# Kernel tuning notes

Hardware: AMD Instinct MI355X
Metric: run time of the kernel (lower is better)

Reference implementation:

```python
import jax, jax.numpy as jnp
import numpy as np

B, S0 = 16, 511
D = 512    # encoder_output_dim
HG = 256   # graph_rnn_hidden_graph
HE = 256   # graph_rnn_hidden_edge (must equal HG: h_prev[0] = graph_state)
T = 128    # tag_representation_dim
M = 32     # graph_rnn_m
S = S0 + 1 # after head-sentinel prepend


def setup_inputs() -> dict:
    ks = iter(jax.random.split(jax.random.key(0), 40))
    def U(shape, fan):
        # torch RNN/Linear default init: U(-1/sqrt(fan), 1/sqrt(fan))
        return jax.random.uniform(next(ks), shape, jnp.float32, -1.0, 1.0) / np.sqrt(fan)
    return {
        'input': jax.random.normal(next(ks), (B, S0, D), jnp.float32),
        'sentinel': jax.random.normal(next(ks), (D,), jnp.float32),
        'g_Wih0': U((HG, D), HG), 'g_Whh0': U((HG, HG), HG), 'g_bih0': U((HG,), HG), 'g_bhh0': U((HG,), HG),
        'g_Wih1': U((HG, HG), HG), 'g_Whh1': U((HG, HG), HG), 'g_bih1': U((HG,), HG), 'g_bhh1': U((HG,), HG),
        'e_Wih0': U((HE, 1), HE), 'e_Whh0': U((HE, HE), HE), 'e_bih0': U((HE,), HE), 'e_bhh0': U((HE,), HE),
        'e_Wih1': U((HE, HE), HE), 'e_Whh1': U((HE, HE), HE), 'e_bih1': U((HE,), HE), 'e_bhh1': U((HE,), HE),
        'cls_W': U((1, HE), HE), 'cls_b': U((1,), HE),
        'head_W': U((T, HG), HG), 'head_b': U((T,), HG),
        'dep_W': U((T, HG), HG), 'dep_b': U((T,), HG),
        'mask': jnp.ones((B, S0), jnp.int32),
        'head_indices': jax.random.randint(next(ks), (B, S0), 0, S0, jnp.int32),
    }


def _rnn_layer(x, W_ih, W_hh, b_ih, b_hh):
    # Elman RNN layer (tanh), batch_first, h0 = 0. x: [B, S, Din] -> [B, S, H]
    xw = jnp.einsum('bsd,hd->bsh', x, W_ih) + b_ih + b_hh  # hoist input GEMM out of scan
    h0 = jnp.zeros((x.shape[0], W_hh.shape[0]), x.dtype)
    def step(h, xw_t):
        h = jnp.tanh(xw_t + h @ W_hh.T)
        return h, h
    _, ys = jax.lax.scan(step, h0, jnp.swapaxes(xw, 0, 1))
    return jnp.swapaxes(ys, 0, 1)


def _forward(input, sentinel, g_Wih0, g_Whh0, g_bih0, g_bhh0, g_Wih1, g_Whh1, g_bih1, g_bhh1,
             e_Wih0, e_Whh0, e_bih0, e_bhh0, e_Wih1, e_Whh1, e_bih1, e_bhh1,
             cls_W, cls_b, head_W, head_b, dep_W, dep_b, mask, head_indices):
    Bv = input.shape[0]
    # prepend head sentinel / prepend_ones
    x = jnp.concatenate([jnp.broadcast_to(sentinel, (Bv, 1, D)), input], axis=1)   # [B,S,D]
    mask_f = jnp.concatenate([jnp.ones((Bv, 1), mask.dtype), mask], axis=1)        # [B,S]
    # graph_pass: 2-layer tanh RNN; pad_packed_sequence zeroes padded timesteps
    h = _rnn_layer(x, g_Wih0, g_Whh0, g_bih0, g_bhh0)
    gs = _rnn_layer(h, g_Wih1, g_Whh1, g_bih1, g_bhh1)                             # [B,S,HG]
    gs = gs * mask_f[..., None].astype(gs.dtype)
    N = Bv * S
    gt = gs.reshape(N, HG)
    def estep(carry, _):
        xe, h0, h1 = carry
        h0 = jnp.tanh(xe @ e_Wih0.T + e_bih0 + e_bhh0 + h0 @ e_Whh0.T)
        h1 = jnp.tanh(h0 @ e_Wih1.T + e_bih1 + e_bhh1 + h1 @ e_Whh1.T)
        p = jax.nn.sigmoid(h1 @ cls_W.T + cls_b)   # [N,1]
        return (p, h0, h1), p[:, 0]
    init = (jnp.ones((N, 1), gs.dtype), gt, jnp.zeros((N, HE), gs.dtype))
    _, probs = jax.lax.scan(estep, init, None, length=M)                           # [M,N]
    A = jnp.concatenate([jnp.ones((1, N), gs.dtype), probs], axis=0).T.reshape(Bv, S, M + 1)
    # reshape_adj: scatter the M-band back into a [B,S,S] matrix, then transpose
    Ab = A[:, :, 1:]                                                               # [B,S,M]
    i = jnp.arange(S)[:, None]
    j = jnp.arange(S)[None, :]
    start = jnp.maximum(0, i - M)
    valid = (j >= start) & (j < i)
    midx = jnp.clip(j - start, 0, M - 1)                                           # [S,S]
    gathered = Ab[:, jnp.arange(S)[:, None], midx]                                 # [B,S,S]
    arc_logits = jnp.swapaxes(jnp.where(valid[None], gathered, jnp.zeros((), gs.dtype)), 1, 2)
    # tag heads (dropout = identity at inference)
    head_tag = jax.nn.elu(jnp.einsum('bsh,th->bst', gs, head_W) + head_b)
    dep_tag = jax.nn.elu(jnp.einsum('bsh,th->bst', gs, dep_W) + dep_b)
    return head_tag, dep_tag, arc_logits


def reference(input, sentinel, g_Wih0, g_Whh0, g_bih0, g_bhh0, g_Wih1, g_Whh1, g_bih1, g_bhh1,
              e_Wih0, e_Whh0, e_bih0, e_bhh0, e_Wih1, e_Whh1, e_bih1, e_bhh1,
              cls_W, cls_b, head_W, head_b, dep_W, dep_b, mask, head_indices):
    return _forward(input, sentinel, g_Wih0, g_Whh0, g_bih0, g_bhh0, g_Wih1, g_Whh1, g_bih1, g_bhh1,
                    e_Wih0, e_Whh0, e_bih0, e_bhh0, e_Wih1, e_Whh1, e_bih1, e_bhh1,
                    cls_W, cls_b, head_W, head_b, dep_W, dep_b, mask, head_indices)
```

## Files before the change

kernel.cpp:

```cpp
#include <hip/hip_runtime.h>

typedef unsigned short u16;
typedef short s8v __attribute__((ext_vector_type(8)));
typedef float f4v __attribute__((ext_vector_type(4)));

__device__ __forceinline__ float bf2f(u16 s) {
  unsigned u = ((unsigned)s) << 16;
  return __builtin_bit_cast(float, u);
}
__device__ __forceinline__ u16 f2bf(float f) {
  unsigned u = __builtin_bit_cast(unsigned, f);
  unsigned r = u + 0x7fffu + ((u >> 16) & 1u);
  return (u16)(r >> 16);
}
__device__ __forceinline__ s8v load8bf(const u16* p) {
  return __builtin_bit_cast(s8v, *(const uint4*)p);
}
__device__ __forceinline__ f4v mfma16(s8v a, s8v b, f4v c) {
  return __builtin_amdgcn_mfma_f32_16x16x32_bf16(a, b, c, 0, 0, 0);
}
__device__ __forceinline__ s8v pin8(s8v x) {
  union { s8v v; unsigned u[4]; } t;
  t.v = x;
  asm volatile("" : "+v"(t.u[0]), "+v"(t.u[1]), "+v"(t.u[2]), "+v"(t.u[3]));
  return t.v;
}
__device__ __forceinline__ void barrier_lds() {
  asm volatile("s_waitcnt lgkmcnt(0)\n\ts_barrier" ::: "memory");
}
__device__ __forceinline__ void cvt8(const float* p, s8v& hi, s8v& lo) {
  float4 x0 = ((const float4*)p)[0];
  float4 x1 = ((const float4*)p)[1];
  float v[8] = {x0.x, x0.y, x0.z, x0.w, x1.x, x1.y, x1.z, x1.w};
  union { s8v v; u16 a[8]; } H, L;
#pragma unroll
  for (int i = 0; i < 8; ++i) {
    u16 h = f2bf(v[i]);
    H.a[i] = h;
    L.a[i] = f2bf(v[i] - bf2f(h));
  }
  hi = H.v;
  lo = L.v;
}
__device__ __forceinline__ float fast_tanh(float x) {
  float t = __builtin_amdgcn_exp2f(x * 2.885390081777927f);
  return 1.f - 2.f * __builtin_amdgcn_rcpf(t + 1.f);
}
__device__ __forceinline__ float fast_sigmoid(float x) {
  float t = __builtin_amdgcn_exp2f(x * -1.4426950408889634f);
  return __builtin_amdgcn_rcpf(1.f + t);
}

__global__ void k_prep(const float* __restrict__ W0, const float* __restrict__ W1,
                       u16* __restrict__ whh0b, u16* __restrict__ whh1b,
                       const float* __restrict__ E0, const float* __restrict__ E1,
                       const float* __restrict__ E2, u16* __restrict__ B0,
                       u16* __restrict__ B1, u16* __restrict__ B2,
                       const float* __restrict__ gW0, u16* __restrict__ gw0hi,
                       u16* __restrict__ gw0lo, const float* __restrict__ gW1,
                       u16* __restrict__ gw1hi, u16* __restrict__ gw1lo,
                       const float* __restrict__ hW, u16* __restrict__ hWhi,
                       u16* __restrict__ hWlo, const float* __restrict__ dW,
                       u16* __restrict__ dWhi, u16* __restrict__ dWlo,
                       const int* __restrict__ mask, float* __restrict__ maskfb) {
  int t = blockIdx.x * 256 + threadIdx.x;
  if (t < 131072) {
    int layer = t >> 16;
    int idx = t & 65535;
    const float* W = layer ? W1 : W0;
    u16* dst = layer ? whh1b : whh0b;
    dst[idx] = f2bf(W[idx]);
  } else if (t < 327680) {
    int c = t - 131072;
    int which = c >> 16;
    int idx = c & 65535;
    const float* src = which == 0 ? E0 : (which == 1 ? E1 : E2);
    u16* dst = which == 0 ? B0 : (which == 1 ? B1 : B2);
    dst[idx] = f2bf(src[idx]);
  } else if (t < 589824) {
    const float* src;
    u16 *dhi, *dlo;
    int idx;
    if (t < 458752) { idx = t - 327680; src = gW0; dhi = gw0hi; dlo = gw0lo; }
    else if (t < 524288) { idx = t - 458752; src = gW1; dhi = gw1hi; dlo = gw1lo; }
    else if (t < 557056) { idx = t - 524288; src = hW; dhi = hWhi; dlo = hWlo; }
    else { idx = t - 557056; src = dW; dhi = dWhi; dlo = dWlo; }
    float v = src[idx];
    u16 h = f2bf(v);
    dhi[idx] = h;
    dlo[idx] = f2bf(v - bf2f(h));
  } else if (t < 598016) {
    int c = t - 589824;
    int s = c >> 4, b = c & 15;
    maskfb[c] = (s == 0) ? 1.f : (float)mask[b * 511 + s - 1];
  }
}

__launch_bounds__(256)
__global__ void k_xw0(const float* __restrict__ input, const float* __restrict__ sentinel,
                      const u16* __restrict__ Whi, const u16* __restrict__ Wlo,
                      const float* __restrict__ b1, const float* __restrict__ b2,
                      float* __restrict__ outxw) {
  const int l = threadIdx.x & 63;
  const int wv = threadIdx.x >> 6;
  const int l15 = l & 15, q = l >> 4;
  const int row0 = blockIdx.x * 64 + wv * 16;
  const int col0 = blockIdx.y * 64;
  int row = row0 + l15;
  int s = row & 511, b = row >> 9;
  const float* aptr = (s == 0) ? sentinel : input + (((size_t)(b * 511 + s - 1)) << 9);
  f4v acc[4];
#pragma unroll
  for (int i = 0; i < 4; ++i) acc[i] = (f4v){0.f, 0.f, 0.f, 0.f};
#pragma unroll
  for (int kt = 0; kt < 16; ++kt) {
    int k0 = kt * 32 + q * 8;
    s8v ah, al;
    cvt8(aptr + k0, ah, al);
#pragma unroll
    for (int nt = 0; nt < 4; ++nt) {
      int j = col0 + nt * 16 + l15;
      s8v wh = load8bf(Whi + ((size_t)j << 9) + k0);
      s8v wl = load8bf(Wlo + ((size_t)j << 9) + k0);
      acc[nt] = mfma16(ah, wh, acc[nt]);
      acc[nt] = mfma16(al, wh, acc[nt]);
      acc[nt] = mfma16(ah, wl, acc[nt]);
    }
  }
#pragma unroll
  for (int nt = 0; nt < 4; ++nt) {
    int col = col0 + nt * 16 + l15;
    float bias = b1[col] + b2[col];
#pragma unroll
    for (int r = 0; r < 4; ++r) {
      int rr = row0 + q * 4 + r;
      outxw[((size_t)rr << 8) + col] = acc[nt][r] + bias;
    }
  }
}

__launch_bounds__(256)
__global__ void k_gemm2(const float* __restrict__ A,
                        const u16* __restrict__ WhiA, const u16* __restrict__ WloA,
                        const float* __restrict__ bA, float* __restrict__ outA,
                        const u16* __restrict__ WhiB, const u16* __restrict__ WloB,
                        const float* __restrict__ bB, float* __restrict__ outB,
                        int K, int J) {
  const u16* Whi = blockIdx.z ? WhiB : WhiA;
  const u16* Wlo = blockIdx.z ? WloB : WloA;
  const float* b1 = blockIdx.z ? bB : bA;
  float* outf = blockIdx.z ? outB : outA;
  const int l = threadIdx.x & 63;
  const int wv = threadIdx.x >> 6;
  const int l15 = l & 15, q = l >> 4;
  const int row0 = blockIdx.x * 64 + wv * 16;
  const int col0 = blockIdx.y * 64;
  const float* aptr = A + (size_t)(row0 + l15) * K;
  f4v acc[4];
#pragma unroll
  for (int i = 0; i < 4; ++i) acc[i] = (f4v){0.f, 0.f, 0.f, 0.f};
  const int nkt = K >> 5;
  for (int kt = 0; kt < nkt; ++kt) {
    int k0 = kt * 32 + q * 8;
    s8v ah, al;
    cvt8(aptr + k0, ah, al);
#pragma unroll
    for (int nt = 0; nt < 4; ++nt) {
      int j = col0 + nt * 16 + l15;
      s8v wh = load8bf(Whi + (size_t)j * K + k0);
      s8v wl = load8bf(Wlo + (size_t)j * K + k0);
      acc[nt] = mfma16(ah, wh, acc[nt]);
      acc[nt] = mfma16(al, wh, acc[nt]);
      acc[nt] = mfma16(ah, wl, acc[nt]);
    }
  }
#pragma unroll
  for (int nt = 0; nt < 4; ++nt) {
    int col = col0 + nt * 16 + l15;
    float bias = b1[col];
#pragma unroll
    for (int r = 0; r < 4; ++r) {
      int rr = row0 + q * 4 + r;
      float v = acc[nt][r] + bias;
      v = v > 0.f ? v : (__builtin_amdgcn_exp2f(v * 1.4426950408889634f) - 1.f);
      outf[(size_t)rr * J + col] = v;
    }
  }
}

__launch_bounds__(512, 2)
__global__ void k_scan_f(const float* __restrict__ xw, const u16* __restrict__ W0b,
                         const u16* __restrict__ Wxb, const u16* __restrict__ W1b,
                         const float* __restrict__ bih1, const float* __restrict__ bhh1,
                         float* __restrict__ outf, const float* __restrict__ maskf) {
  __shared__ u16 H1[2][272];
  __shared__ u16 H2[2][272];
  __shared__ float XW2[2][272];
  __shared__ float mtab[512];
  const int tid = threadIdx.x;
  const int l = tid & 63, wv = tid >> 6;
  const int l15 = l & 15, q = l >> 4;
  const int b = blockIdx.x;

  s8v w0[2][8], wx[2][8], w1[2][8];
#pragma unroll
  for (int nt = 0; nt < 2; ++nt) {
    int j = wv * 32 + nt * 16 + l15;
#pragma unroll
    for (int kt = 0; kt < 8; ++kt) {
      int off = (j << 8) + kt * 32 + q * 8;
      w0[nt][kt] = pin8(load8bf(W0b + off));
      wx[nt][kt] = pin8(load8bf(Wxb + off));
      w1[nt][kt] = pin8(load8bf(W1b + off));
    }
  }
  if (tid < 256) {
    H1[0][tid] = 0; H1[1][tid] = 0;
    H2[0][tid] = 0; H2[1][tid] = 0;
    XW2[0][tid] = 0.f; XW2[1][tid] = 0.f;
  }
  if (tid < 512) mtab[tid] = maskf[tid * 16 + b];

  const int j0 = wv * 32 + l15;
  float b2v[2];
#pragma unroll
  for (int nt = 0; nt < 2; ++nt) b2v[nt] = bih1[j0 + nt * 16] + bhh1[j0 + nt * 16];
  __syncthreads();

  const size_t nbase = (size_t)b << 9;
  const float* xrow = xw + (nbase << 8);
  const int q0 = (q == 0);

  float xA[2], xB[2];
#pragma unroll
  for (int nt = 0; nt < 2; ++nt) {
    xA[nt] = xrow[j0 + nt * 16];
    xB[nt] = xrow[256 + j0 + nt * 16];
  }

  auto STEP = [&](int g, int par, float* xc) {
    const u16* H1r = &H1[par][0];
    const u16* H2r = &H2[par][0];
    f4v a1[2], ax[2], a2[2], a2b[2];
#pragma unroll
    for (int nt = 0; nt < 2; ++nt) {
      a1[nt] = (f4v){xc[nt], 0.f, 0.f, 0.f};
      ax[nt] = (f4v){b2v[nt], 0.f, 0.f, 0.f};
      a2[nt] = (f4v){XW2[par][j0 + nt * 16], 0.f, 0.f, 0.f};
      a2b[nt] = (f4v){0.f, 0.f, 0.f, 0.f};
    }
#pragma unroll
    for (int kt = 0; kt < 8; ++kt) {
      s8v h1b = load8bf(H1r + kt * 32 + q * 8);
#pragma unroll
      for (int nt = 0; nt < 2; ++nt) {
        a1[nt] = mfma16(h1b, w0[nt][kt], a1[nt]);
        ax[nt] = mfma16(h1b, wx[nt][kt], ax[nt]);
      }
    }
    if (g < 512) {
      u16* Hw = &H1[1 - par][0];
#pragma unroll
      for (int nt = 0; nt < 2; ++nt) {
        float h = fast_tanh(a1[nt][0]);
        if (q0) Hw[j0 + nt * 16] = f2bf(h);
      }
    }
    if (g >= 1 && g < 513) {
      float* Xw = &XW2[1 - par][0];
#pragma unroll
      for (int nt = 0; nt < 2; ++nt)
        if (q0) Xw[j0 + nt * 16] = ax[nt][0];
    }
#pragma unroll
    for (int kt = 0; kt < 8; ++kt) {
      s8v h2b = load8bf(H2r + kt * 32 + q * 8);
#pragma unroll
      for (int nt = 0; nt < 2; ++nt) {
        if (kt & 1) a2b[nt] = mfma16(h2b, w1[nt][kt], a2b[nt]);
        else        a2[nt]  = mfma16(h2b, w1[nt][kt], a2[nt]);
      }
    }
    if (g >= 2) {
      int t = g - 2;
      float mf = mtab[t];
      u16* Hw = &H2[1 - par][0];
      float* orow = outf + ((nbase + t) << 8);
#pragma unroll
      for (int nt = 0; nt < 2; ++nt) {
        float h = fast_tanh(a2[nt][0] + a2b[nt][0]);
        if (q0) {
          Hw[j0 + nt * 16] = f2bf(h);
          orow[j0 + nt * 16] = h * mf;
        }
      }
    }
  };

  for (int g = 0; g < 514; g += 2) {
    STEP(g, 0, xA);
    int sp = g + 2; if (sp > 511) sp = 511;
#pragma unroll
    for (int nt = 0; nt < 2; ++nt) xA[nt] = xrow[(sp << 8) + j0 + nt * 16];
    barrier_lds();
    STEP(g + 1, 1, xB);
    int sq = g + 3; if (sq > 511) sq = 511;
#pragma unroll
    for (int nt = 0; nt < 2; ++nt) xB[nt] = xrow[(sq << 8) + j0 + nt * 16];
    barrier_lds();
  }
}

__launch_bounds__(512, 2)
__global__ void k_enc(const float* __restrict__ gs,
                      const u16* __restrict__ W0b, const u16* __restrict__ W1b,
                      const u16* __restrict__ W2b, const float* __restrict__ wih0,
                      const float* __restrict__ bih0, const float* __restrict__ bhh0,
                      const float* __restrict__ bih1, const float* __restrict__ bhh1,
                      const float* __restrict__ clsW, const float* __restrict__ clsb,
                      float* __restrict__ Ab) {
  __shared__ __align__(16) u16 hA0[32 * 264];
  __shared__ __align__(16) u16 hA1[32 * 264];
  __shared__ float xe[32];
  __shared__ float b0v[256], w0v[256], b1v[256], clsv[256];
  __shared__ float clsbs;
  const int tid = threadIdx.x;
  const int n0 = blockIdx.x * 32;

  for (int c = tid; c < 8192; c += 512) {
    int row = c >> 8, col = c & 255;
    hA0[row * 264 + col] = f2bf(gs[(((size_t)(n0 + row)) << 8) + col]);
    hA1[row * 264 + col] = 0;
  }
  if (tid < 256) {
    b0v[tid] = bih0[tid] + bhh0[tid];
    w0v[tid] = wih0[tid];
    b1v[tid] = bih1[tid] + bhh1[tid];
    clsv[tid] = clsW[tid];
  }
  if (tid < 32) xe[tid] = 1.0f;
  if (tid == 0) clsbs = clsb[0];

  const int l = tid & 63, wv = tid >> 6;
  const int l15 = l & 15, q = l >> 4;
  const int colbase = wv * 32;

  s8v w0[2][8], w1[2][8], w2[2][8];
#pragma unroll
  for (int nt = 0; nt < 2; ++nt) {
    int jj = colbase + nt * 16 + l15;
#pragma unroll
    for (int kt = 0; kt < 8; ++kt) {
      int off = (jj << 8) + kt * 32 + q * 8;
      w0[nt][kt] = load8bf(W0b + off);
      w1[nt][kt] = load8bf(W1b + off);
      w2[nt][kt] = load8bf(W2b + off);
    }
  }
  __syncthreads();

  for (int m = 0; m < 32; ++m) {
    f4v acc[2][2];
#pragma unroll
    for (int mt = 0; mt < 2; ++mt)
#pragma unroll
      for (int nt = 0; nt < 2; ++nt) acc[mt][nt] = (f4v){0.f, 0.f, 0.f, 0.f};
#pragma unroll
    for (int kt = 0; kt < 8; ++kt) {
#pragma unroll
      for (int mt = 0; mt < 2; ++mt) {
        s8v a = __builtin_bit_cast(s8v, *(const uint4*)&hA0[(mt * 16 + l15) * 264 + kt * 32 + q * 8]);
        acc[mt][0] = mfma16(a, w0[0][kt], acc[mt][0]);
        acc[mt][1] = mfma16(a, w0[1][kt], acc[mt][1]);
      }
    }
    __syncthreads();
#pragma unroll
    for (int nt = 0; nt < 2; ++nt) {
      int col = colbase + nt * 16 + l15;
      float wc = w0v[col], bc = b0v[col];
#pragma unroll
      for (int mt = 0; mt < 2; ++mt)
#pragma unroll
        for (int r = 0; r < 4; ++r) {
          int row = mt * 16 + q * 4 + r;
          float v = acc[mt][nt][r] + xe[row] * wc + bc;
          hA0[row * 264 + col] = f2bf(fast_tanh(v));
        }
    }
    __syncthreads();
#pragma unroll
    for (int mt = 0; mt < 2; ++mt)
#pragma unroll
      for (int nt = 0; nt < 2; ++nt) acc[mt][nt] = (f4v){0.f, 0.f, 0.f, 0.f};
#pragma unroll
    for (int kt = 0; kt < 8; ++kt) {
#pragma unroll
      for (int mt = 0; mt < 2; ++mt) {
        s8v a0 = __builtin_bit_cast(s8v, *(const uint4*)&hA0[(mt * 16 + l15) * 264 + kt * 32 + q * 8]);
        s8v a1 = __builtin_bit_cast(s8v, *(const uint4*)&hA1[(mt * 16 + l15) * 264 + kt * 32 + q * 8]);
        acc[mt][0] = mfma16(a0, w1[0][kt], acc[mt][0]);
        acc[mt][1] = mfma16(a0, w1[1][kt], acc[mt][1]);
        acc[mt][0] = mfma16(a1, w2[0][kt], acc[mt][0]);
        acc[mt][1] = mfma16(a1, w2[1][kt], acc[mt][1]);
      }
    }
    __syncthreads();
#pragma unroll
    for (int nt = 0; nt < 2; ++nt) {
      int col = colbase + nt * 16 + l15;
      float bc = b1v[col];
#pragma unroll
      for (int mt = 0; mt < 2; ++mt)
#pragma unroll
        for (int r = 0; r < 4; ++r) {
          int row = mt * 16 + q * 4 + r;
          float v = acc[mt][nt][r] + bc;
          hA1[row * 264 + col] = f2bf(fast_tanh(v));
        }
    }
    __syncthreads();
    if (tid < 256) {
      int row = tid >> 3, seg = tid & 7;
      float sum = 0.f;
#pragma unroll
      for (int u = 0; u < 4; ++u) {
        int col = seg * 32 + u * 8;
#pragma unroll
        for (int e = 0; e < 8; ++e) sum += bf2f(hA1[row * 264 + col + e]) * clsv[col + e];
      }
      sum += __shfl_down(sum, 4, 8);
      sum += __shfl_down(sum, 2, 8);
      sum += __shfl_down(sum, 1, 8);
      if (seg == 0) {
        float pp = fast_sigmoid(sum + clsbs);
        xe[row] = pp;
        Ab[(((size_t)(n0 + row)) << 5) + m] = pp;
      }
    }
    __syncthreads();
  }
}

__global__ void k_arc(const float* __restrict__ Ab, float* __restrict__ out2) {
  int t = blockIdx.x * 256 + threadIdx.x;
  int b = t >> 18;
  int rem = t & 262143;
  int j = rem >> 9, i = rem & 511;
  int start = i - 32;
  if (start < 0) start = 0;
  float v = 0.f;
  if (j >= start && j < i) v = Ab[((((size_t)b << 9) + i) << 5) + (j - start)];
  out2[t] = v;
}

extern "C" void kernel_launch(void* const* d_in, const int* in_sizes, int n_in,
                              void* d_out, int out_size, void* d_ws, size_t ws_size,
                              hipStream_t stream) {
  const float* input    = (const float*)d_in[0];
  const float* sentinel = (const float*)d_in[1];
  const float* g_Wih0   = (const float*)d_in[2];
  const float* g_Whh0   = (const float*)d_in[3];
  const float* g_bih0   = (const float*)d_in[4];
  const float* g_bhh0   = (const float*)d_in[5];
  const float* g_Wih1   = (const float*)d_in[6];
  const float* g_Whh1   = (const float*)d_in[7];
  const float* g_bih1   = (const float*)d_in[8];
  const float* g_bhh1   = (const float*)d_in[9];
  const float* e_Wih0   = (const float*)d_in[10];
  const float* e_Whh0   = (const float*)d_in[11];
  const float* e_bih0   = (const float*)d_in[12];
  const float* e_bhh0   = (const float*)d_in[13];
  const float* e_Wih1   = (const float*)d_in[14];
  const float* e_Whh1   = (const float*)d_in[15];
  const float* e_bih1   = (const float*)d_in[16];
  const float* e_bhh1   = (const float*)d_in[17];
  const float* cls_W    = (const float*)d_in[18];
  const float* cls_b    = (const float*)d_in[19];
  const float* head_W   = (const float*)d_in[20];
  const float* head_b   = (const float*)d_in[21];
  const float* dep_W    = (const float*)d_in[22];
  const float* dep_b    = (const float*)d_in[23];
  const int* mask       = (const int*)d_in[24];

  float* out = (float*)d_out;
  char* ws = (char*)d_ws;
  float* xw_buf = (float*)ws;
  float* gsb    = (float*)(ws + (16u << 20));
  float* Ab     = (float*)(ws + (24u << 20));
  size_t o = (25u << 20);
  u16* whh0b   = (u16*)(ws + o); o += 128u << 10;
  u16* whh1b   = (u16*)(ws + o); o += 128u << 10;
  float* maskfb= (float*)(ws + o); o += 32u << 10;
  u16* eb0     = (u16*)(ws + o); o += 128u << 10;
  u16* eb1     = (u16*)(ws + o); o += 128u << 10;
  u16* eb2     = (u16*)(ws + o); o += 128u << 10;
  u16* gw0hi   = (u16*)(ws + o); o += 256u << 10;
  u16* gw0lo   = (u16*)(ws + o); o += 256u << 10;
  u16* gw1hi   = (u16*)(ws + o); o += 128u << 10;
  u16* gw1lo   = (u16*)(ws + o); o += 128u << 10;
  u16* hWhi    = (u16*)(ws + o); o += 64u << 10;
  u16* hWlo    = (u16*)(ws + o); o += 64u << 10;
  u16* dWhi    = (u16*)(ws + o); o += 64u << 10;
  u16* dWlo    = (u16*)(ws + o); o += 64u << 10;

  k_prep<<<2336, 256, 0, stream>>>(g_Whh0, g_Whh1, whh0b, whh1b, e_Whh0, e_Wih1, e_Whh1,
                                   eb0, eb1, eb2, g_Wih0, gw0hi, gw0lo, g_Wih1, gw1hi,
                                   gw1lo, head_W, hWhi, hWlo, dep_W, dWhi, dWlo,
                                   mask, maskfb);
  k_xw0<<<dim3(128, 4), 256, 0, stream>>>(input, sentinel, gw0hi, gw0lo, g_bih0, g_bhh0,
                                          xw_buf);
  k_scan_f<<<16, 512, 0, stream>>>(xw_buf, whh0b, gw1hi, whh1b, g_bih1, g_bhh1,
                                   gsb, maskfb);
  k_gemm2<<<dim3(128, 2, 2), 256, 0, stream>>>(gsb, hWhi, hWlo, head_b, out,
                                               dWhi, dWlo, dep_b, out + 1048576,
                                               256, 128);
  k_enc<<<256, 512, 0, stream>>>(gsb, eb0, eb1, eb2, e_Wih0, e_bih0, e_bhh0,
                                 e_bih1, e_bhh1, cls_W, cls_b, Ab);
  k_arc<<<16384, 256, 0, stream>>>(Ab, out + 2097152);
}
```

Before: 867.7 us.

## Replace MFMA matvec in graph RNN scan with fp16 dot2 lane-pair reductions

```diff
diff --git a/kernel.cpp b/kernel.cpp
--- a/kernel.cpp
+++ b/kernel.cpp
@@ -3,6 +3,9 @@
 typedef unsigned short u16;
 typedef short s8v __attribute__((ext_vector_type(8)));
 typedef float f4v __attribute__((ext_vector_type(4)));
+typedef _Float16 f16;
+typedef _Float16 h2v __attribute__((ext_vector_type(2)));
+typedef _Float16 h8v __attribute__((ext_vector_type(8)));
 
 __device__ __forceinline__ float bf2f(u16 s) {
   unsigned u = ((unsigned)s) << 16;
@@ -19,14 +22,27 @@
 __device__ __forceinline__ f4v mfma16(s8v a, s8v b, f4v c) {
   return __builtin_amdgcn_mfma_f32_16x16x32_bf16(a, b, c, 0, 0, 0);
 }
-__device__ __forceinline__ s8v pin8(s8v x) {
-  union { s8v v; unsigned u[4]; } t;
+__device__ __forceinline__ h8v pinh(h8v x) {
+  union { h8v v; unsigned u[4]; } t;
   t.v = x;
   asm volatile("" : "+v"(t.u[0]), "+v"(t.u[1]), "+v"(t.u[2]), "+v"(t.u[3]));
   return t.v;
 }
 __device__ __forceinline__ void barrier_lds() {
   asm volatile("s_waitcnt lgkmcnt(0)\n\ts_barrier" ::: "memory");
+}
+__device__ __forceinline__ float swz_xor1(float x) {
+  int i = __builtin_bit_cast(int, x);
+  i = __builtin_amdgcn_ds_swizzle(i, 0x041F);
+  return __builtin_bit_cast(float, i);
+}
+__device__ __forceinline__ h2v pr(h8v v, int e) {
+  union { h8v v; h2v p[4]; } t;
+  t.v = v;
+  return t.p[e];
+}
+__device__ __forceinline__ float fdot2(h2v a, h2v b, float c) {
+  return __builtin_amdgcn_fdot2(a, b, c, false);
 }
 __device__ __forceinline__ void cvt8(const float* p, s8v& hi, s8v& lo) {
   float4 x0 = ((const float4*)p)[0];
@@ -51,27 +67,27 @@
   return __builtin_amdgcn_rcpf(1.f + t);
 }
 
-__global__ void k_prep(const float* __restrict__ W0, const float* __restrict__ W1,
-                       u16* __restrict__ whh0b, u16* __restrict__ whh1b,
+__global__ void k_prep(const float* __restrict__ W0, const float* __restrict__ Wx,
+                       const float* __restrict__ W1, f16* __restrict__ w0h,
+                       f16* __restrict__ wxh, f16* __restrict__ w1h,
                        const float* __restrict__ E0, const float* __restrict__ E1,
                        const float* __restrict__ E2, u16* __restrict__ B0,
                        u16* __restrict__ B1, u16* __restrict__ B2,
                        const float* __restrict__ gW0, u16* __restrict__ gw0hi,
-                       u16* __restrict__ gw0lo, const float* __restrict__ gW1,
-                       u16* __restrict__ gw1hi, u16* __restrict__ gw1lo,
+                       u16* __restrict__ gw0lo,
                        const float* __restrict__ hW, u16* __restrict__ hWhi,
                        u16* __restrict__ hWlo, const float* __restrict__ dW,
                        u16* __restrict__ dWhi, u16* __restrict__ dWlo,
                        const int* __restrict__ mask, float* __restrict__ maskfb) {
   int t = blockIdx.x * 256 + threadIdx.x;
-  if (t < 131072) {
-    int layer = t >> 16;
+  if (t < 196608) {
+    int which = t >> 16;
     int idx = t & 65535;
-    const float* W = layer ? W1 : W0;
-    u16* dst = layer ? whh1b : whh0b;
-    dst[idx] = f2bf(W[idx]);
-  } else if (t < 327680) {
-    int c = t - 131072;
+    const float* src = which == 0 ? W0 : (which == 1 ? Wx : W1);
+    f16* dst = which == 0 ? w0h : (which == 1 ? wxh : w1h);
+    dst[idx] = (f16)src[idx];
+  } else if (t < 393216) {
+    int c = t - 196608;
     int which = c >> 16;
     int idx = c & 65535;
     const float* src = which == 0 ? E0 : (which == 1 ? E1 : E2);
@@ -81,8 +97,7 @@
     const float* src;
     u16 *dhi, *dlo;
     int idx;
-    if (t < 458752) { idx = t - 327680; src = gW0; dhi = gw0hi; dlo = gw0lo; }
-    else if (t < 524288) { idx = t - 458752; src = gW1; dhi = gw1hi; dlo = gw1lo; }
+    if (t < 524288) { idx = t - 393216; src = gW0; dhi = gw0hi; dlo = gw0lo; }
     else if (t < 557056) { idx = t - 524288; src = hW; dhi = hWhi; dlo = hWlo; }
     else { idx = t - 557056; src = dW; dhi = dWhi; dlo = dWlo; }
     float v = src[idx];
@@ -189,124 +204,110 @@
 }
 
 __launch_bounds__(512, 2)
-__global__ void k_scan_f(const float* __restrict__ xw, const u16* __restrict__ W0b,
-                         const u16* __restrict__ Wxb, const u16* __restrict__ W1b,
+__global__ void k_scan_d(const float* __restrict__ xw, const f16* __restrict__ W0h,
+                         const f16* __restrict__ Wxh, const f16* __restrict__ W1h,
                          const float* __restrict__ bih1, const float* __restrict__ bhh1,
                          float* __restrict__ outf, const float* __restrict__ maskf) {
-  __shared__ u16 H1[2][272];
-  __shared__ u16 H2[2][272];
-  __shared__ float XW2[2][272];
+  __shared__ f16 H1[2][256];
+  __shared__ f16 H2[2][256];
+  __shared__ float XW2[2][256];
   __shared__ float mtab[512];
   const int tid = threadIdx.x;
   const int l = tid & 63, wv = tid >> 6;
-  const int l15 = l & 15, q = l >> 4;
+  const int jw = l >> 1, p = l & 1;
+  const int j = wv * 32 + jw;
   const int b = blockIdx.x;
 
-  s8v w0[2][8], wx[2][8], w1[2][8];
-#pragma unroll
-  for (int nt = 0; nt < 2; ++nt) {
-    int j = wv * 32 + nt * 16 + l15;
-#pragma unroll
-    for (int kt = 0; kt < 8; ++kt) {
-      int off = (j << 8) + kt * 32 + q * 8;
-      w0[nt][kt] = pin8(load8bf(W0b + off));
-      wx[nt][kt] = pin8(load8bf(Wxb + off));
-      w1[nt][kt] = pin8(load8bf(W1b + off));
+  h8v w0[16], wx[16], w1[16];
+  {
+    const size_t base = ((size_t)j << 8) + (p << 7);
+#pragma unroll
+    for (int i = 0; i < 16; ++i) {
+      w0[i] = pinh(*(const h8v*)(W0h + base + i * 8));
+      wx[i] = pinh(*(const h8v*)(Wxh + base + i * 8));
+      w1[i] = pinh(*(const h8v*)(W1h + base + i * 8));
     }
   }
   if (tid < 256) {
-    H1[0][tid] = 0; H1[1][tid] = 0;
-    H2[0][tid] = 0; H2[1][tid] = 0;
+    H1[0][tid] = (f16)0.f; H1[1][tid] = (f16)0.f;
+    H2[0][tid] = (f16)0.f; H2[1][tid] = (f16)0.f;
     XW2[0][tid] = 0.f; XW2[1][tid] = 0.f;
   }
   if (tid < 512) mtab[tid] = maskf[tid * 16 + b];
-
-  const int j0 = wv * 32 + l15;
-  float b2v[2];
-#pragma unroll
-  for (int nt = 0; nt < 2; ++nt) b2v[nt] = bih1[j0 + nt * 16] + bhh1[j0 + nt * 16];
+  const float b2v = bih1[j] + bhh1[j];
   __syncthreads();
 
   const size_t nbase = (size_t)b << 9;
   const float* xrow = xw + (nbase << 8);
-  const int q0 = (q == 0);
-
-  float xA[2], xB[2];
-#pragma unroll
-  for (int nt = 0; nt < 2; ++nt) {
-    xA[nt] = xrow[j0 + nt * 16];
-    xB[nt] = xrow[256 + j0 + nt * 16];
-  }
-
-  auto STEP = [&](int g, int par, float* xc) {
-    const u16* H1r = &H1[par][0];
-    const u16* H2r = &H2[par][0];
-    f4v a1[2], ax[2], a2[2], a2b[2];
-#pragma unroll
-    for (int nt = 0; nt < 2; ++nt) {
-      a1[nt] = (f4v){xc[nt], 0.f, 0.f, 0.f};
-      ax[nt] = (f4v){b2v[nt], 0.f, 0.f, 0.f};
-      a2[nt] = (f4v){XW2[par][j0 + nt * 16], 0.f, 0.f, 0.f};
-      a2b[nt] = (f4v){0.f, 0.f, 0.f, 0.f};
-    }
-#pragma unroll
-    for (int kt = 0; kt < 8; ++kt) {
-      s8v h1b = load8bf(H1r + kt * 32 + q * 8);
-#pragma unroll
-      for (int nt = 0; nt < 2; ++nt) {
-        a1[nt] = mfma16(h1b, w0[nt][kt], a1[nt]);
-        ax[nt] = mfma16(h1b, wx[nt][kt], ax[nt]);
-      }
-    }
-    if (g < 512) {
-      u16* Hw = &H1[1 - par][0];
-#pragma unroll
-      for (int nt = 0; nt < 2; ++nt) {
-        float h = fast_tanh(a1[nt][0]);
-        if (q0) Hw[j0 + nt * 16] = f2bf(h);
-      }
-    }
-    if (g >= 1 && g < 513) {
-      float* Xw = &XW2[1 - par][0];
-#pragma unroll
-      for (int nt = 0; nt < 2; ++nt)
-        if (q0) Xw[j0 + nt * 16] = ax[nt][0];
-    }
-#pragma unroll
-    for (int kt = 0; kt < 8; ++kt) {
-      s8v h2b = load8bf(H2r + kt * 32 + q * 8);
-#pragma unroll
-      for (int nt = 0; nt < 2; ++nt) {
-        if (kt & 1) a2b[nt] = mfma16(h2b, w1[nt][kt], a2b[nt]);
-        else        a2[nt]  = mfma16(h2b, w1[nt][kt], a2[nt]);
-      }
+  const int hoff = p << 7;
+
+  float xA = xrow[j], xB = xrow[256 + j];
+
+  auto STEP = [&](int g, int par, float xc) {
+    const f16* H1r = &H1[par][0] + hoff;
+    const f16* H2r = &H2[par][0] + hoff;
+    float xwprev = XW2[par][j];
+    float s1a = 0.f, s1b = 0.f, sxa = 0.f, sxb = 0.f;
+    float s2[4] = {0.f, 0.f, 0.f, 0.f};
+#pragma unroll
+    for (int c = 0; c < 4; ++c) {
+      h8v h[4];
+#pragma unroll
+      for (int u = 0; u < 4; ++u) h[u] = *(const h8v*)(H1r + c * 32 + u * 8);
+#pragma unroll
+      for (int u = 0; u < 4; ++u)
+#pragma unroll
+        for (int e = 0; e < 4; ++e) {
+          h2v hp = pr(h[u], e);
+          if (e & 1) {
+            s1b = fdot2(hp, pr(w0[c * 4 + u], e), s1b);
+            sxb = fdot2(hp, pr(wx[c * 4 + u], e), sxb);
+          } else {
+            s1a = fdot2(hp, pr(w0[c * 4 + u], e), s1a);
+            sxa = fdot2(hp, pr(wx[c * 4 + u], e), sxa);
+          }
+        }
+    }
+#pragma unroll
+    for (int c = 0; c < 4; ++c) {
+      h8v h[4];
+#pragma unroll
+      for (int u = 0; u < 4; ++u) h[u] = *(const h8v*)(H2r + c * 32 + u * 8);
+#pragma unroll
+      for (int u = 0; u < 4; ++u)
+#pragma unroll
+        for (int e = 0; e < 4; ++e)
+          s2[e] = fdot2(pr(h[u], e), pr(w1[c * 4 + u], e), s2[e]);
+    }
+    float t1 = s1a + s1b, tx = sxa + sxb;
+    float t2 = (s2[0] + s2[1]) + (s2[2] + s2[3]);
+    t1 += swz_xor1(t1);
+    tx += swz_xor1(tx);
+    t2 += swz_xor1(t2);
+    float h1n = fast_tanh(xc + t1);
+    float xwn = b2v + tx;
+    if (p == 0) {
+      H1[1 - par][j] = (f16)h1n;
+      XW2[1 - par][j] = xwn;
     }
     if (g >= 2) {
       int t = g - 2;
-      float mf = mtab[t];
-      u16* Hw = &H2[1 - par][0];
-      float* orow = outf + ((nbase + t) << 8);
-#pragma unroll
-      for (int nt = 0; nt < 2; ++nt) {
-        float h = fast_tanh(a2[nt][0] + a2b[nt][0]);
-        if (q0) {
-          Hw[j0 + nt * 16] = f2bf(h);
-          orow[j0 + nt * 16] = h * mf;
-        }
+      float h2n = fast_tanh(xwprev + t2);
+      if (p == 0) {
+        H2[1 - par][j] = (f16)h2n;
+        outf[((nbase + (size_t)t) << 8) + j] = h2n * mtab[t];
       }
     }
   };
 
   for (int g = 0; g < 514; g += 2) {
     STEP(g, 0, xA);
-    int sp = g + 2; if (sp > 511) sp = 511;
-#pragma unroll
-    for (int nt = 0; nt < 2; ++nt) xA[nt] = xrow[(sp << 8) + j0 + nt * 16];
+    int sp = g + 2 > 511 ? 511 : g + 2;
+    xA = xrow[(sp << 8) + j];
     barrier_lds();
     STEP(g + 1, 1, xB);
-    int sq = g + 3; if (sq > 511) sq = 511;
-#pragma unroll
-    for (int nt = 0; nt < 2; ++nt) xB[nt] = xrow[(sq << 8) + j0 + nt * 16];
+    int sq = g + 3 > 511 ? 511 : g + 3;
+    xB = xrow[(sq << 8) + j];
     barrier_lds();
   }
 }
@@ -489,28 +490,27 @@
   float* gsb    = (float*)(ws + (16u << 20));
   float* Ab     = (float*)(ws + (24u << 20));
   size_t o = (25u << 20);
-  u16* whh0b   = (u16*)(ws + o); o += 128u << 10;
-  u16* whh1b   = (u16*)(ws + o); o += 128u << 10;
+  f16* w0h     = (f16*)(ws + o); o += 128u << 10;
+  f16* wxh     = (f16*)(ws + o); o += 128u << 10;
+  f16* w1h     = (f16*)(ws + o); o += 128u << 10;
   float* maskfb= (float*)(ws + o); o += 32u << 10;
   u16* eb0     = (u16*)(ws + o); o += 128u << 10;
   u16* eb1     = (u16*)(ws + o); o += 128u << 10;
   u16* eb2     = (u16*)(ws + o); o += 128u << 10;
   u16* gw0hi   = (u16*)(ws + o); o += 256u << 10;
   u16* gw0lo   = (u16*)(ws + o); o += 256u << 10;
-  u16* gw1hi   = (u16*)(ws + o); o += 128u << 10;
-  u16* gw1lo   = (u16*)(ws + o); o += 128u << 10;
   u16* hWhi    = (u16*)(ws + o); o += 64u << 10;
   u16* hWlo    = (u16*)(ws + o); o += 64u << 10;
   u16* dWhi    = (u16*)(ws + o); o += 64u << 10;
   u16* dWlo    = (u16*)(ws + o); o += 64u << 10;
 
-  k_prep<<<2336, 256, 0, stream>>>(g_Whh0, g_Whh1, whh0b, whh1b, e_Whh0, e_Wih1, e_Whh1,
-                                   eb0, eb1, eb2, g_Wih0, gw0hi, gw0lo, g_Wih1, gw1hi,
-                                   gw1lo, head_W, hWhi, hWlo, dep_W, dWhi, dWlo,
-                                   mask, maskfb);
+  k_prep<<<2336, 256, 0, stream>>>(g_Whh0, g_Wih1, g_Whh1, w0h, wxh, w1h,
+                                   e_Whh0, e_Wih1, e_Whh1, eb0, eb1, eb2,
+                                   g_Wih0, gw0hi, gw0lo, head_W, hWhi, hWlo,
+                                   dep_W, dWhi, dWlo, mask, maskfb);
   k_xw0<<<dim3(128, 4), 256, 0, stream>>>(input, sentinel, gw0hi, gw0lo, g_bih0, g_bhh0,
                                           xw_buf);
-  k_scan_f<<<16, 512, 0, stream>>>(xw_buf, whh0b, gw1hi, whh1b, g_bih1, g_bhh1,
+  k_scan_d<<<16, 512, 0, stream>>>(xw_buf, w0h, wxh, w1h, g_bih1, g_bhh1,
                                    gsb, maskfb);
   k_gemm2<<<dim3(128, 2, 2), 256, 0, stream>>>(gsb, hWhi, hWlo, head_b, out,
                                                dWhi, dWlo, dep_b, out + 1048576,
```

Result: slower. 959.1 us (+10.5%).

## Process two batch sequences per block in the recurrent scan kernel

Applied to the files above, without the earlier changes.

```diff
diff --git a/kernel.cpp b/kernel.cpp
--- a/kernel.cpp
+++ b/kernel.cpp
@@ -193,14 +193,14 @@
                          const u16* __restrict__ Wxb, const u16* __restrict__ W1b,
                          const float* __restrict__ bih1, const float* __restrict__ bhh1,
                          float* __restrict__ outf, const float* __restrict__ maskf) {
-  __shared__ u16 H1[2][272];
-  __shared__ u16 H2[2][272];
-  __shared__ float XW2[2][272];
-  __shared__ float mtab[512];
+  __shared__ u16 H1[2][2][272];
+  __shared__ u16 H2[2][2][272];
+  __shared__ float XW2[2][2][272];
+  __shared__ float mtab[2][512];
   const int tid = threadIdx.x;
   const int l = tid & 63, wv = tid >> 6;
   const int l15 = l & 15, q = l >> 4;
-  const int b = blockIdx.x;
+  const int bi = blockIdx.x;
 
   s8v w0[2][8], wx[2][8], w1[2][8];
 #pragma unroll
@@ -215,11 +215,17 @@
     }
   }
   if (tid < 256) {
-    H1[0][tid] = 0; H1[1][tid] = 0;
-    H2[0][tid] = 0; H2[1][tid] = 0;
-    XW2[0][tid] = 0.f; XW2[1][tid] = 0.f;
-  }
-  if (tid < 512) mtab[tid] = maskf[tid * 16 + b];
+#pragma unroll
+    for (int r = 0; r < 2; ++r) {
+      H1[r][0][tid] = 0; H1[r][1][tid] = 0;
+      H2[r][0][tid] = 0; H2[r][1][tid] = 0;
+      XW2[r][0][tid] = 0.f; XW2[r][1][tid] = 0.f;
+    }
+  }
+  for (int c = tid; c < 1024; c += 512) {
+    int r = c >> 9, s = c & 511;
+    mtab[r][s] = maskf[s * 16 + 2 * bi + r];
+  }
 
   const int j0 = wv * 32 + l15;
   float b2v[2];
@@ -227,86 +233,110 @@
   for (int nt = 0; nt < 2; ++nt) b2v[nt] = bih1[j0 + nt * 16] + bhh1[j0 + nt * 16];
   __syncthreads();
 
-  const size_t nbase = (size_t)b << 9;
-  const float* xrow = xw + (nbase << 8);
+  const size_t nbaseA = (size_t)(2 * bi) << 9;
+  const size_t nbaseB = (size_t)(2 * bi + 1) << 9;
+  const float* xrowA = xw + (nbaseA << 8);
+  const float* xrowB = xw + (nbaseB << 8);
   const int q0 = (q == 0);
 
-  float xA[2], xB[2];
+  float xE[2][2], xO[2][2];
 #pragma unroll
   for (int nt = 0; nt < 2; ++nt) {
-    xA[nt] = xrow[j0 + nt * 16];
-    xB[nt] = xrow[256 + j0 + nt * 16];
-  }
-
-  auto STEP = [&](int g, int par, float* xc) {
-    const u16* H1r = &H1[par][0];
-    const u16* H2r = &H2[par][0];
-    f4v a1[2], ax[2], a2[2], a2b[2];
-#pragma unroll
-    for (int nt = 0; nt < 2; ++nt) {
-      a1[nt] = (f4v){xc[nt], 0.f, 0.f, 0.f};
-      ax[nt] = (f4v){b2v[nt], 0.f, 0.f, 0.f};
-      a2[nt] = (f4v){XW2[par][j0 + nt * 16], 0.f, 0.f, 0.f};
-      a2b[nt] = (f4v){0.f, 0.f, 0.f, 0.f};
-    }
+    xE[0][nt] = xrowA[j0 + nt * 16];
+    xE[1][nt] = xrowB[j0 + nt * 16];
+    xO[0][nt] = xrowA[256 + j0 + nt * 16];
+    xO[1][nt] = xrowB[256 + j0 + nt * 16];
+  }
+
+  auto STEP = [&](int g, int par, float (*xc)[2]) {
+    const u16* H1r[2] = {&H1[0][par][0], &H1[1][par][0]};
+    const u16* H2r[2] = {&H2[0][par][0], &H2[1][par][0]};
+    f4v a1[2][2], ax[2][2], a2[2][2];
+#pragma unroll
+    for (int r = 0; r < 2; ++r)
+#pragma unroll
+      for (int nt = 0; nt < 2; ++nt) {
+        a1[r][nt] = (f4v){xc[r][nt], 0.f, 0.f, 0.f};
+        ax[r][nt] = (f4v){b2v[nt], 0.f, 0.f, 0.f};
+        a2[r][nt] = (f4v){XW2[r][par][j0 + nt * 16], 0.f, 0.f, 0.f};
+      }
 #pragma unroll
     for (int kt = 0; kt < 8; ++kt) {
-      s8v h1b = load8bf(H1r + kt * 32 + q * 8);
+      s8v hA = load8bf(H1r[0] + kt * 32 + q * 8);
+      s8v hB = load8bf(H1r[1] + kt * 32 + q * 8);
 #pragma unroll
       for (int nt = 0; nt < 2; ++nt) {
-        a1[nt] = mfma16(h1b, w0[nt][kt], a1[nt]);
-        ax[nt] = mfma16(h1b, wx[nt][kt], ax[nt]);
+        a1[0][nt] = mfma16(hA, w0[nt][kt], a1[0][nt]);
+        ax[0][nt] = mfma16(hA, wx[nt][kt], ax[0][nt]);
+        a1[1][nt] = mfma16(hB, w0[nt][kt], a1[1][nt]);
+        ax[1][nt] = mfma16(hB, wx[nt][kt], ax[1][nt]);
+      }
+    }
+#pragma unroll
+    for (int kt = 0; kt < 8; ++kt) {
+      s8v hA = load8bf(H2r[0] + kt * 32 + q * 8);
+      s8v hB = load8bf(H2r[1] + kt * 32 + q * 8);
+#pragma unroll
+      for (int nt = 0; nt < 2; ++nt) {
+        a2[0][nt] = mfma16(hA, w1[nt][kt], a2[0][nt]);
+        a2[1][nt] = mfma16(hB, w1[nt][kt], a2[1][nt]);
       }
     }
     if (g < 512) {
-      u16* Hw = &H1[1 - par][0];
-#pragma unroll
-      for (int nt = 0; nt < 2; ++nt) {
-        float h = fast_tanh(a1[nt][0]);
-        if (q0) Hw[j0 + nt * 16] = f2bf(h);
+#pragma unroll
+      for (int r = 0; r < 2; ++r) {
+        u16* Hw = &H1[r][1 - par][0];
+#pragma unroll
+        for (int nt = 0; nt < 2; ++nt) {
+          float h = fast_tanh(a1[r][nt][0]);
+          if (q0) Hw[j0 + nt * 16] = f2bf(h);
+        }
       }
     }
     if (g >= 1 && g < 513) {
-      float* Xw = &XW2[1 - par][0];
-#pragma unroll
-      for (int nt = 0; nt < 2; ++nt)
-        if (q0) Xw[j0 + nt * 16] = ax[nt][0];
-    }
-#pragma unroll
-    for (int kt = 0; kt < 8; ++kt) {
-      s8v h2b = load8bf(H2r + kt * 32 + q * 8);
-#pragma unroll
-      for (int nt = 0; nt < 2; ++nt) {
-        if (kt & 1) a2b[nt] = mfma16(h2b, w1[nt][kt], a2b[nt]);
-        else        a2[nt]  = mfma16(h2b, w1[nt][kt], a2[nt]);
+#pragma unroll
+      for (int r = 0; r < 2; ++r) {
+        float* Xw = &XW2[r][1 - par][0];
+#pragma unroll
+        for (int nt = 0; nt < 2; ++nt)
+          if (q0) Xw[j0 + nt * 16] = ax[r][nt][0];
       }
     }
     if (g >= 2) {
       int t = g - 2;
-      float mf = mtab[t];
-      u16* Hw = &H2[1 - par][0];
-      float* orow = outf + ((nbase + t) << 8);
-#pragma unroll
-      for (int nt = 0; nt < 2; ++nt) {
-        float h = fast_tanh(a2[nt][0] + a2b[nt][0]);
-        if (q0) {
-          Hw[j0 + nt * 16] = f2bf(h);
-          orow[j0 + nt * 16] = h * mf;
+      float* orow[2] = {outf + ((nbaseA + t) << 8), outf + ((nbaseB + t) << 8)};
+#pragma unroll
+      for (int r = 0; r < 2; ++r) {
+        float mf = mtab[r][t];
+        u16* Hw = &H2[r][1 - par][0];
+#pragma unroll
+        for (int nt = 0; nt < 2; ++nt) {
+          float h = fast_tanh(a2[r][nt][0]);
+          if (q0) {
+            Hw[j0 + nt * 16] = f2bf(h);
+            orow[r][j0 + nt * 16] = h * mf;
+          }
         }
       }
     }
   };
 
   for (int g = 0; g < 514; g += 2) {
-    STEP(g, 0, xA);
+    STEP(g, 0, xE);
     int sp = g + 2; if (sp > 511) sp = 511;
 #pragma unroll
-    for (int nt = 0; nt < 2; ++nt) xA[nt] = xrow[(sp << 8) + j0 + nt * 16];
+    for (int nt = 0; nt < 2; ++nt) {
+      xE[0][nt] = xrowA[(sp << 8) + j0 + nt * 16];
+      xE[1][nt] = xrowB[(sp << 8) + j0 + nt * 16];
+    }
     barrier_lds();
-    STEP(g + 1, 1, xB);
+    STEP(g + 1, 1, xO);
     int sq = g + 3; if (sq > 511) sq = 511;
 #pragma unroll
-    for (int nt = 0; nt < 2; ++nt) xB[nt] = xrow[(sq << 8) + j0 + nt * 16];
+    for (int nt = 0; nt < 2; ++nt) {
+      xO[0][nt] = xrowA[(sq << 8) + j0 + nt * 16];
+      xO[1][nt] = xrowB[(sq << 8) + j0 + nt * 16];
+    }
     barrier_lds();
   }
 }
@@ -510,8 +540,8 @@
                                    mask, maskfb);
   k_xw0<<<dim3(128, 4), 256, 0, stream>>>(input, sentinel, gw0hi, gw0lo, g_bih0, g_bhh0,
                                           xw_buf);
-  k_scan_f<<<16, 512, 0, stream>>>(xw_buf, whh0b, gw1hi, whh1b, g_bih1, g_bhh1,
-                                   gsb, maskfb);
+  k_scan_f<<<8, 512, 0, stream>>>(xw_buf, whh0b, gw1hi, whh1b, g_bih1, g_bhh1,
+                                  gsb, maskfb);
   k_gemm2<<<dim3(128, 2, 2), 256, 0, stream>>>(gsb, hWhi, hWlo, head_b, out,
                                                dWhi, dWlo, dep_b, out + 1048576,
                                                256, 128);
```

After: 1.740 ms. +100.6%, slower.
